# Kernel optimization log

Measured on AMD Instinct MI355X. Metric: run time of the kernel, lower is better.

## Reference

```python
import jax, jax.numpy as jnp
import numpy as np

B, S, D, H = 4, 2048, 1024, 16
HD = D // H


def setup_inputs() -> dict:
    key = jax.random.key(0)
    ks = jax.random.split(key, 12)
    sc = 1.0 / np.sqrt(D)
    return {
        "x": jax.random.normal(ks[0], (B, S, D), dtype=jnp.float32),
        "key_padding_mask": jax.random.randint(ks[1], (B, S), 0, 2).astype(bool),
        "attn_mask_modifier": jax.random.uniform(ks[2], (B, S, S), dtype=jnp.float32),
        "Wq": jax.random.normal(ks[3], (D, D), dtype=jnp.float32) * sc,
        "bq": jax.random.normal(ks[4], (D,), dtype=jnp.float32) * sc,
        "Wk": jax.random.normal(ks[5], (D, D), dtype=jnp.float32) * sc,
        "bk": jax.random.normal(ks[6], (D,), dtype=jnp.float32) * sc,
        "Wv": jax.random.normal(ks[7], (D, D), dtype=jnp.float32) * sc,
        "bv": jax.random.normal(ks[8], (D,), dtype=jnp.float32) * sc,
        "Wo": jax.random.normal(ks[9], (D, D), dtype=jnp.float32) * sc,
        "bo": jax.random.normal(ks[10], (D,), dtype=jnp.float32) * sc,
    }


def reference(x, key_padding_mask, attn_mask_modifier, Wq, bq, Wk, bk, Wv, bv, Wo, bo):
    b, s, d = x.shape
    hd = d // H
    # QKV projections -> [b, H, s, hd]
    q = (x @ Wq + bq).reshape(b, s, H, hd).transpose(0, 2, 1, 3)
    k = (x @ Wk + bk).reshape(b, s, H, hd).transpose(0, 2, 1, 3)
    v = (x @ Wv + bv).reshape(b, s, H, hd).transpose(0, 2, 1, 3)
    energy = jnp.einsum("bhqd,bhkd->bhqk", q, k) / jnp.sqrt(jnp.asarray(hd, x.dtype))
    # handle_neg=False path: multiplicative mask modifier, broadcast over heads
    energy = energy * attn_mask_modifier[:, None, :, :]
    # key_padding_mask is applied on the QUERY axis (unsqueeze(1).unsqueeze(-1)) per source
    energy = jnp.where(key_padding_mask[:, None, :, None], jnp.asarray(-1e10, x.dtype), energy)
    attn = jax.nn.softmax(energy, axis=-1)
    out = jnp.einsum("bhqk,bhkd->bhqd", attn, v).transpose(0, 2, 1, 3).reshape(b, s, d)
    return out @ Wo + bo
```

## Files before the change

### kernel.cpp

```cpp
#include <hip/hip_runtime.h>
#include <cstddef>

constexpr int Bn  = 4;
constexpr int Sn  = 2048;
constexpr int Dn  = 1024;
constexpr int Hn  = 16;
constexpr int HDn = 64;

typedef __bf16 bf16;
typedef __attribute__((ext_vector_type(8))) __bf16 bf16x8;
typedef __attribute__((ext_vector_type(4))) __bf16 bf16x4;
typedef __attribute__((ext_vector_type(4))) float  f32x4;

typedef __attribute__((address_space(1))) const void gvoid;
typedef __attribute__((address_space(3))) void lvoid;

__global__ __launch_bounds__(256) void conv_f32_bf16_k(
    const float* __restrict__ in, bf16* __restrict__ out, int n)
{
    int i = (blockIdx.x * 256 + threadIdx.x) * 4;
    if (i + 3 < n) {
        float4 v = *(const float4*)(in + i);
        bf16 o[4] = {(bf16)v.x, (bf16)v.y, (bf16)v.z, (bf16)v.w};
        *(ulong1*)(out + i) = *(ulong1*)o;
    }
}

__global__ __launch_bounds__(256) void conv_wt_k(
    const float* __restrict__ w0, const float* __restrict__ w1,
    const float* __restrict__ w2, const float* __restrict__ w3,
    bf16* __restrict__ o0, bf16* __restrict__ o1,
    bf16* __restrict__ o2, bf16* __restrict__ o3)
{
    const float* W = (blockIdx.z == 0) ? w0 : (blockIdx.z == 1) ? w1
                   : (blockIdx.z == 2) ? w2 : w3;
    bf16* O = (blockIdx.z == 0) ? o0 : (blockIdx.z == 1) ? o1
            : (blockIdx.z == 2) ? o2 : o3;
    __shared__ float t[64][65];
    const int tid = threadIdx.x;
    const int k0 = blockIdx.x * 64;
    const int n0 = blockIdx.y * 64;
    #pragma unroll
    for (int p = 0; p < 16; ++p) {
        const int idx = p * 256 + tid;
        const int r = idx >> 6, c = idx & 63;
        t[r][c] = W[(size_t)(k0 + r) * Dn + n0 + c];
    }
    __syncthreads();
    #pragma unroll
    for (int p = 0; p < 16; ++p) {
        const int idx = p * 256 + tid;
        const int r = idx >> 6, c = idx & 63;
        O[(size_t)(n0 + r) * Dn + k0 + c] = (bf16)t[c][r];
    }
}

template <int MODE>
__global__ __launch_bounds__(256) void gemm_bf16_k(
    const bf16* __restrict__ A, const bf16* __restrict__ Bt,
    const float* __restrict__ bias, void* __restrict__ outv)
{
    __shared__ __align__(16) bf16 As[128 * 64];
    __shared__ __align__(16) bf16 Bs[128 * 64];

    const int tid  = threadIdx.x;
    const int w    = tid >> 6;
    const int lane = tid & 63;
    const int quad = lane >> 4;
    const int l15  = lane & 15;
    const int m0   = blockIdx.x * 128;
    const int n0   = blockIdx.y * 128;
    const int wm   = w >> 1;
    const int wn   = w & 1;

    const int srow = lane >> 3;
    const int scol = (lane & 7) * 8;

    f32x4 acc[4][4] = {};

    for (int k0 = 0; k0 < Dn; k0 += 64) {
        #pragma unroll
        for (int j = 0; j < 4; ++j) {
            const int rbase = (w * 4 + j) * 8;
            const int r = rbase + srow;
            __builtin_amdgcn_global_load_lds(
                (gvoid*)(A + (size_t)(m0 + r) * Dn + k0 + scol),
                (lvoid*)&As[rbase * 64], 16, 0, 0);
            __builtin_amdgcn_global_load_lds(
                (gvoid*)(Bt + (size_t)(n0 + r) * Dn + k0 + scol),
                (lvoid*)&Bs[rbase * 64], 16, 0, 0);
        }
        __syncthreads();

        #pragma unroll
        for (int ks = 0; ks < 64; ks += 32) {
            bf16x8 af[4], bfr[4];
            #pragma unroll
            for (int fm = 0; fm < 4; ++fm)
                af[fm] = *(const bf16x8*)&As[(wm * 64 + fm * 16 + l15) * 64 + ks + quad * 8];
            #pragma unroll
            for (int fn = 0; fn < 4; ++fn)
                bfr[fn] = *(const bf16x8*)&Bs[(wn * 64 + fn * 16 + l15) * 64 + ks + quad * 8];
            #pragma unroll
            for (int fm = 0; fm < 4; ++fm)
                #pragma unroll
                for (int fn = 0; fn < 4; ++fn)
                    acc[fm][fn] = __builtin_amdgcn_mfma_f32_16x16x32_bf16(
                        af[fm], bfr[fn], acc[fm][fn], 0, 0, 0);
        }
        __syncthreads();
    }

    #pragma unroll
    for (int fn = 0; fn < 4; ++fn) {
        const int c = n0 + wn * 64 + fn * 16 + l15;
        const float bv = bias[c];
        #pragma unroll
        for (int fm = 0; fm < 4; ++fm) {
            #pragma unroll
            for (int i = 0; i < 4; ++i) {
                const int m = m0 + wm * 64 + fm * 16 + quad * 4 + i;
                const float v = acc[fm][fn][i] + bv;
                if (MODE == 0) {
                    ((float*)outv)[(size_t)m * Dn + c] = v;
                } else {
                    const int b = m >> 11, s = m & (Sn - 1);
                    const int h = c >> 6, hd = c & 63;
                    if (MODE == 1)
                        ((bf16*)outv)[(((size_t)(b * Hn + h) * Sn) + s) * HDn + hd] = (bf16)v;
                    else
                        ((bf16*)outv)[(((size_t)(b * Hn + h) * HDn) + hd) * Sn + s] = (bf16)v;
                }
            }
        }
    }
}

__device__ __forceinline__ int sidx(int r, int c) {
    return r * 64 + (c ^ ((r & 7) << 3));
}

__global__ __launch_bounds__(256) void attn_mfma_k(
    const bf16* __restrict__ Qb, const bf16* __restrict__ Kb,
    const bf16* __restrict__ Vtb, const int* __restrict__ kpm,
    const float* __restrict__ mod, bf16* __restrict__ att)
{
    __shared__ __align__(16) bf16 Ks[64 * 64];
    __shared__ __align__(16) bf16 Vts[64 * 64];
    __shared__ __align__(16) bf16 Ps[64 * 64];

    const int tid  = threadIdx.x;
    const int w    = tid >> 6;
    const int lane = tid & 63;
    const int quad = lane >> 4;
    const int l15  = lane & 15;
    const int blk  = blockIdx.x;
    const int bh   = blk >> 5;
    const int q0   = (blk & 31) * 64;
    const int b    = bh >> 4;
    const int h    = bh & 15;
    const size_t base = (size_t)bh * Sn * HDn;

    const int qrow = q0 + w * 16 + l15;
    const bf16x8 qf0 = *(const bf16x8*)(Qb + base + (size_t)qrow * HDn + 0  + quad * 8);
    const bf16x8 qf1 = *(const bf16x8*)(Qb + base + (size_t)qrow * HDn + 32 + quad * 8);

    const bool qm = kpm[(size_t)b * Sn + qrow] != 0;
    const float* modrow = mod + ((size_t)b * Sn + qrow) * Sn;

    constexpr float SC = 0.125f * 1.44269504088896340736f;

    float m_r = -1e30f;
    float l_r = 0.0f;
    f32x4 O[4] = {};

    int sr[2], soff[2];
    #pragma unroll
    for (int p = 0; p < 2; ++p) {
        const int c = p * 256 + tid;
        sr[p] = c >> 3; soff[p] = (c & 7) * 8;
    }

    bf16x8 kst[2], vst[2];
    float4 md[4];
    #pragma unroll
    for (int p = 0; p < 2; ++p) {
        kst[p] = *(const bf16x8*)(Kb + base + (size_t)sr[p] * HDn + soff[p]);
        vst[p] = *(const bf16x8*)(Vtb + base + (size_t)sr[p] * Sn + 0 + soff[p]);
    }
    #pragma unroll
    for (int ct = 0; ct < 4; ++ct)
        md[ct] = *(const float4*)(modrow + 0 + ct * 16 + quad * 4);
    #pragma unroll
    for (int p = 0; p < 2; ++p) {
        *(bf16x8*)&Ks[sidx(sr[p], soff[p])]  = kst[p];
        *(bf16x8*)&Vts[sidx(sr[p], soff[p])] = vst[p];
    }
    __syncthreads();

    constexpr int NT = Sn / 64;
    for (int t = 0; t < NT; ++t) {
        const int k0 = t * 64;

        float4 mdn[4];
        if (t + 1 < NT) {
            const int kn = k0 + 64;
            #pragma unroll
            for (int p = 0; p < 2; ++p) {
                kst[p] = *(const bf16x8*)(Kb + base + (size_t)(kn + sr[p]) * HDn + soff[p]);
                vst[p] = *(const bf16x8*)(Vtb + base + (size_t)sr[p] * Sn + kn + soff[p]);
            }
            #pragma unroll
            for (int ct = 0; ct < 4; ++ct)
                mdn[ct] = *(const float4*)(modrow + kn + ct * 16 + quad * 4);
        }

        float e[4][4];
        #pragma unroll
        for (int ct = 0; ct < 4; ++ct) {
            f32x4 s = {};
            #pragma unroll
            for (int ks = 0; ks < 64; ks += 32) {
                bf16x8 kf = *(const bf16x8*)&Ks[sidx(ct * 16 + l15, ks + quad * 8)];
                s = __builtin_amdgcn_mfma_f32_16x16x32_bf16(kf, ks ? qf1 : qf0, s, 0, 0, 0);
            }
            #pragma unroll
            for (int i = 0; i < 4; ++i)
                e[ct][i] = qm ? -1e10f : s[i] * SC * (&md[ct].x)[i];
        }

        float pmax = e[0][0];
        #pragma unroll
        for (int ct = 0; ct < 4; ++ct)
            #pragma unroll
            for (int i = 0; i < 4; ++i)
                pmax = fmaxf(pmax, e[ct][i]);
        pmax = fmaxf(pmax, __shfl_xor(pmax, 16));
        pmax = fmaxf(pmax, __shfl_xor(pmax, 32));

        const float mnew  = fmaxf(m_r, pmax);
        const float alpha = __builtin_amdgcn_exp2f(m_r - mnew);
        m_r = mnew;

        float rs = 0.0f;
        #pragma unroll
        for (int ct = 0; ct < 4; ++ct) {
            bf16x4 pb;
            #pragma unroll
            for (int i = 0; i < 4; ++i) {
                const bf16 p = (bf16)__builtin_amdgcn_exp2f(e[ct][i] - mnew);
                pb[i] = p;
                rs += (float)p;
            }
            *(bf16x4*)&Ps[sidx(w * 16 + l15, ct * 16 + quad * 4)] = pb;
        }
        rs += __shfl_xor(rs, 16);
        rs += __shfl_xor(rs, 32);
        l_r = l_r * alpha + rs;

        float aO[4];
        #pragma unroll
        for (int i = 0; i < 4; ++i)
            aO[i] = __shfl(alpha, quad * 4 + i, 16);
        #pragma unroll
        for (int ct = 0; ct < 4; ++ct)
            #pragma unroll
            for (int i = 0; i < 4; ++i)
                O[ct][i] *= aO[i];

        #pragma unroll
        for (int ks = 0; ks < 64; ks += 32) {
            bf16x8 paf = *(const bf16x8*)&Ps[sidx(w * 16 + l15, ks + quad * 8)];
            #pragma unroll
            for (int ct = 0; ct < 4; ++ct) {
                bf16x8 vf = *(const bf16x8*)&Vts[sidx(ct * 16 + l15, ks + quad * 8)];
                O[ct] = __builtin_amdgcn_mfma_f32_16x16x32_bf16(paf, vf, O[ct], 0, 0, 0);
            }
        }

        __syncthreads();
        if (t + 1 < NT) {
            #pragma unroll
            for (int p = 0; p < 2; ++p) {
                *(bf16x8*)&Ks[sidx(sr[p], soff[p])]  = kst[p];
                *(bf16x8*)&Vts[sidx(sr[p], soff[p])] = vst[p];
            }
            #pragma unroll
            for (int ct = 0; ct < 4; ++ct)
                md[ct] = mdn[ct];
        }
        __syncthreads();
    }

    float lO[4];
    #pragma unroll
    for (int i = 0; i < 4; ++i)
        lO[i] = 1.0f / __shfl(l_r, quad * 4 + i, 16);
    #pragma unroll
    for (int ct = 0; ct < 4; ++ct)
        #pragma unroll
        for (int i = 0; i < 4; ++i) {
            const int row = q0 + w * 16 + quad * 4 + i;
            const int col = h * HDn + ct * 16 + l15;
            att[((size_t)b * Sn + row) * Dn + col] = (bf16)(O[ct][i] * lO[i]);
        }
}

extern "C" void kernel_launch(void* const* d_in, const int* in_sizes, int n_in,
                              void* d_out, int out_size, void* d_ws, size_t ws_size,
                              hipStream_t stream) {
    const float* x   = (const float*)d_in[0];
    const int*   kpm = (const int*)d_in[1];
    const float* mod = (const float*)d_in[2];
    const float* Wq  = (const float*)d_in[3];
    const float* bq  = (const float*)d_in[4];
    const float* Wk  = (const float*)d_in[5];
    const float* bk  = (const float*)d_in[6];
    const float* Wv  = (const float*)d_in[7];
    const float* bv  = (const float*)d_in[8];
    const float* Wo  = (const float*)d_in[9];
    const float* bo  = (const float*)d_in[10];
    float* out = (float*)d_out;

    bf16* ws = (bf16*)d_ws;
    const size_t sz = (size_t)Bn * Sn * Dn;
    const size_t wz = (size_t)Dn * Dn;
    bf16* xb   = ws;
    bf16* qb   = ws + sz;
    bf16* kb   = ws + 2 * sz;
    bf16* vtb  = ws + 3 * sz;
    bf16* attb = ws + 4 * sz;
    bf16* wqt  = ws + 5 * sz;
    bf16* wkt  = wqt + wz;
    bf16* wvt  = wkt + wz;
    bf16* wot  = wvt + wz;

    conv_f32_bf16_k<<<(int)(sz / 1024), 256, 0, stream>>>(x, xb, (int)sz);
    conv_wt_k<<<dim3(16, 16, 4), 256, 0, stream>>>(Wq, Wk, Wv, Wo, wqt, wkt, wvt, wot);

    const dim3 gemm_grid(64, 8);
    gemm_bf16_k<1><<<gemm_grid, 256, 0, stream>>>(xb, wqt, bq, qb);
    gemm_bf16_k<1><<<gemm_grid, 256, 0, stream>>>(xb, wkt, bk, kb);
    gemm_bf16_k<2><<<gemm_grid, 256, 0, stream>>>(xb, wvt, bv, vtb);

    attn_mfma_k<<<Bn * Hn * (Sn / 64), 256, 0, stream>>>(qb, kb, vtb, kpm, mod, attb);

    gemm_bf16_k<0><<<gemm_grid, 256, 0, stream>>>(attb, wot, bo, out);
}
```

Baseline: 437.4 us.

## Double-buffer attention K/V via direct LDS loads, lazy rescale, fold scale into Q

The attention kernel now double-buffers K and V tiles in LDS, filling them with global_load_lds directly from memory instead of staging through registers, and drops one barrier per iteration. The online softmax rescales O and l only when the running max grows by more than a threshold (a conditional-rescale trick). The softmax scale is folded into the Q projection epilogue. The V-transpose GEMM epilogue now goes through an LDS transpose so global stores are coalesced. Risks: the direct LDS loads are not followed by an explicit vmcnt wait, and the removed barrier may create a race on the Ps buffer and on buffer reuse across iterations.

```diff
diff --git a/kernel.cpp b/kernel.cpp
--- a/kernel.cpp
+++ b/kernel.cpp
@@ -58,10 +58,12 @@
 template <int MODE>
 __global__ __launch_bounds__(256) void gemm_bf16_k(
     const bf16* __restrict__ A, const bf16* __restrict__ Bt,
-    const float* __restrict__ bias, void* __restrict__ outv)
+    const float* __restrict__ bias, void* __restrict__ outv, float scale)
 {
-    __shared__ __align__(16) bf16 As[128 * 64];
-    __shared__ __align__(16) bf16 Bs[128 * 64];
+    constexpr int SM_ELEMS = (MODE == 2) ? (128 * 136) : (2 * 128 * 64);
+    __shared__ __align__(16) bf16 smem[SM_ELEMS];
+    bf16* const As = smem;
+    bf16* const Bs = smem + 128 * 64;
 
     const int tid  = threadIdx.x;
     const int w    = tid >> 6;
@@ -111,25 +113,52 @@
         __syncthreads();
     }
 
-    #pragma unroll
-    for (int fn = 0; fn < 4; ++fn) {
-        const int c = n0 + wn * 64 + fn * 16 + l15;
-        const float bv = bias[c];
-        #pragma unroll
-        for (int fm = 0; fm < 4; ++fm) {
-            #pragma unroll
-            for (int i = 0; i < 4; ++i) {
-                const int m = m0 + wm * 64 + fm * 16 + quad * 4 + i;
-                const float v = acc[fm][fn][i] + bv;
-                if (MODE == 0) {
-                    ((float*)outv)[(size_t)m * Dn + c] = v;
-                } else {
-                    const int b = m >> 11, s = m & (Sn - 1);
-                    const int h = c >> 6, hd = c & 63;
-                    if (MODE == 1)
+    if (MODE == 2) {
+        bf16* const T = smem;
+        #pragma unroll
+        for (int fn = 0; fn < 4; ++fn) {
+            const int n = wn * 64 + fn * 16 + l15;
+            const float bv = bias[n0 + n];
+            #pragma unroll
+            for (int fm = 0; fm < 4; ++fm) {
+                const int m = wm * 64 + fm * 16 + quad * 4;
+                bf16x4 pk;
+                #pragma unroll
+                for (int i = 0; i < 4; ++i)
+                    pk[i] = (bf16)((acc[fm][fn][i] + bv) * scale);
+                *(bf16x4*)&T[n * 136 + m] = pk;
+            }
+        }
+        __syncthreads();
+        const int b  = m0 >> 11;
+        const int s0 = m0 & (Sn - 1);
+        #pragma unroll
+        for (int it = 0; it < 8; ++it) {
+            const int n    = it * 16 + (tid >> 4);
+            const int mcol = (tid & 15) * 8;
+            const int gh = (n0 + n) >> 6, ghd = (n0 + n) & 63;
+            bf16x8 v = *(const bf16x8*)&T[n * 136 + mcol];
+            *(bf16x8*)((bf16*)outv +
+                (((size_t)(b * Hn + gh) * HDn) + ghd) * Sn + s0 + mcol) = v;
+        }
+    } else {
+        #pragma unroll
+        for (int fn = 0; fn < 4; ++fn) {
+            const int c = n0 + wn * 64 + fn * 16 + l15;
+            const float bv = bias[c];
+            #pragma unroll
+            for (int fm = 0; fm < 4; ++fm) {
+                #pragma unroll
+                for (int i = 0; i < 4; ++i) {
+                    const int m = m0 + wm * 64 + fm * 16 + quad * 4 + i;
+                    const float v = (acc[fm][fn][i] + bv) * scale;
+                    if (MODE == 0) {
+                        ((float*)outv)[(size_t)m * Dn + c] = v;
+                    } else {
+                        const int b = m >> 11, s = m & (Sn - 1);
+                        const int h = c >> 6, hd = c & 63;
                         ((bf16*)outv)[(((size_t)(b * Hn + h) * Sn) + s) * HDn + hd] = (bf16)v;
-                    else
-                        ((bf16*)outv)[(((size_t)(b * Hn + h) * HDn) + hd) * Sn + s] = (bf16)v;
+                    }
                 }
             }
         }
@@ -145,8 +174,8 @@
     const bf16* __restrict__ Vtb, const int* __restrict__ kpm,
     const float* __restrict__ mod, bf16* __restrict__ att)
 {
-    __shared__ __align__(16) bf16 Ks[64 * 64];
-    __shared__ __align__(16) bf16 Vts[64 * 64];
+    __shared__ __align__(16) bf16 Ks[2][64 * 64];
+    __shared__ __align__(16) bf16 Vts[2][64 * 64];
     __shared__ __align__(16) bf16 Ps[64 * 64];
 
     const int tid  = threadIdx.x;
@@ -168,51 +197,44 @@
     const bool qm = kpm[(size_t)b * Sn + qrow] != 0;
     const float* modrow = mod + ((size_t)b * Sn + qrow) * Sn;
 
-    constexpr float SC = 0.125f * 1.44269504088896340736f;
-
     float m_r = -1e30f;
     float l_r = 0.0f;
     f32x4 O[4] = {};
 
-    int sr[2], soff[2];
-    #pragma unroll
-    for (int p = 0; p < 2; ++p) {
-        const int c = p * 256 + tid;
-        sr[p] = c >> 3; soff[p] = (c & 7) * 8;
-    }
-
-    bf16x8 kst[2], vst[2];
+    const int rl = lane >> 3;
+    const int cg = ((lane & 7) ^ rl) * 8;
+
+    auto stage = [&](int t, int buf) {
+        const int k0 = t * 64;
+        #pragma unroll
+        for (int p = 0; p < 2; ++p) {
+            const int gb = p * 32 + w * 8;
+            __builtin_amdgcn_global_load_lds(
+                (gvoid*)(Kb + base + (size_t)(k0 + gb + rl) * HDn + cg),
+                (lvoid*)&Ks[buf][gb * 64], 16, 0, 0);
+            __builtin_amdgcn_global_load_lds(
+                (gvoid*)(Vtb + base + (size_t)(gb + rl) * Sn + k0 + cg),
+                (lvoid*)&Vts[buf][gb * 64], 16, 0, 0);
+        }
+    };
+
+    stage(0, 0);
     float4 md[4];
     #pragma unroll
-    for (int p = 0; p < 2; ++p) {
-        kst[p] = *(const bf16x8*)(Kb + base + (size_t)sr[p] * HDn + soff[p]);
-        vst[p] = *(const bf16x8*)(Vtb + base + (size_t)sr[p] * Sn + 0 + soff[p]);
-    }
-    #pragma unroll
     for (int ct = 0; ct < 4; ++ct)
-        md[ct] = *(const float4*)(modrow + 0 + ct * 16 + quad * 4);
-    #pragma unroll
-    for (int p = 0; p < 2; ++p) {
-        *(bf16x8*)&Ks[sidx(sr[p], soff[p])]  = kst[p];
-        *(bf16x8*)&Vts[sidx(sr[p], soff[p])] = vst[p];
-    }
+        md[ct] = *(const float4*)(modrow + ct * 16 + quad * 4);
     __syncthreads();
 
     constexpr int NT = Sn / 64;
     for (int t = 0; t < NT; ++t) {
-        const int k0 = t * 64;
+        const int cur = t & 1;
 
         float4 mdn[4];
         if (t + 1 < NT) {
-            const int kn = k0 + 64;
-            #pragma unroll
-            for (int p = 0; p < 2; ++p) {
-                kst[p] = *(const bf16x8*)(Kb + base + (size_t)(kn + sr[p]) * HDn + soff[p]);
-                vst[p] = *(const bf16x8*)(Vtb + base + (size_t)sr[p] * Sn + kn + soff[p]);
-            }
+            stage(t + 1, cur ^ 1);
             #pragma unroll
             for (int ct = 0; ct < 4; ++ct)
-                mdn[ct] = *(const float4*)(modrow + kn + ct * 16 + quad * 4);
+                mdn[ct] = *(const float4*)(modrow + (t + 1) * 64 + ct * 16 + quad * 4);
         }
 
         float e[4][4];
@@ -221,12 +243,12 @@
             f32x4 s = {};
             #pragma unroll
             for (int ks = 0; ks < 64; ks += 32) {
-                bf16x8 kf = *(const bf16x8*)&Ks[sidx(ct * 16 + l15, ks + quad * 8)];
+                bf16x8 kf = *(const bf16x8*)&Ks[cur][sidx(ct * 16 + l15, ks + quad * 8)];
                 s = __builtin_amdgcn_mfma_f32_16x16x32_bf16(kf, ks ? qf1 : qf0, s, 0, 0, 0);
             }
             #pragma unroll
             for (int i = 0; i < 4; ++i)
-                e[ct][i] = qm ? -1e10f : s[i] * SC * (&md[ct].x)[i];
+                e[ct][i] = qm ? -1e10f : s[i] * (&md[ct].x)[i];
         }
 
         float pmax = e[0][0];
@@ -238,9 +260,21 @@
         pmax = fmaxf(pmax, __shfl_xor(pmax, 16));
         pmax = fmaxf(pmax, __shfl_xor(pmax, 32));
 
-        const float mnew  = fmaxf(m_r, pmax);
-        const float alpha = __builtin_amdgcn_exp2f(m_r - mnew);
-        m_r = mnew;
+        if (__any(pmax > m_r + 8.0f)) {
+            const float mnew  = fmaxf(m_r, pmax);
+            const float alpha = __builtin_amdgcn_exp2f(m_r - mnew);
+            m_r = mnew;
+            l_r *= alpha;
+            float aO[4];
+            #pragma unroll
+            for (int i = 0; i < 4; ++i)
+                aO[i] = __shfl(alpha, quad * 4 + i, 16);
+            #pragma unroll
+            for (int ct = 0; ct < 4; ++ct)
+                #pragma unroll
+                for (int i = 0; i < 4; ++i)
+                    O[ct][i] *= aO[i];
+        }
 
         float rs = 0.0f;
         #pragma unroll
@@ -248,7 +282,7 @@
             bf16x4 pb;
             #pragma unroll
             for (int i = 0; i < 4; ++i) {
-                const bf16 p = (bf16)__builtin_amdgcn_exp2f(e[ct][i] - mnew);
+                const bf16 p = (bf16)__builtin_amdgcn_exp2f(e[ct][i] - m_r);
                 pb[i] = p;
                 rs += (float)p;
             }
@@ -256,35 +290,19 @@
         }
         rs += __shfl_xor(rs, 16);
         rs += __shfl_xor(rs, 32);
-        l_r = l_r * alpha + rs;
-
-        float aO[4];
-        #pragma unroll
-        for (int i = 0; i < 4; ++i)
-            aO[i] = __shfl(alpha, quad * 4 + i, 16);
-        #pragma unroll
-        for (int ct = 0; ct < 4; ++ct)
-            #pragma unroll
-            for (int i = 0; i < 4; ++i)
-                O[ct][i] *= aO[i];
+        l_r += rs;
 
         #pragma unroll
         for (int ks = 0; ks < 64; ks += 32) {
             bf16x8 paf = *(const bf16x8*)&Ps[sidx(w * 16 + l15, ks + quad * 8)];
             #pragma unroll
             for (int ct = 0; ct < 4; ++ct) {
-                bf16x8 vf = *(const bf16x8*)&Vts[sidx(ct * 16 + l15, ks + quad * 8)];
+                bf16x8 vf = *(const bf16x8*)&Vts[cur][sidx(ct * 16 + l15, ks + quad * 8)];
                 O[ct] = __builtin_amdgcn_mfma_f32_16x16x32_bf16(paf, vf, O[ct], 0, 0, 0);
             }
         }
 
-        __syncthreads();
         if (t + 1 < NT) {
-            #pragma unroll
-            for (int p = 0; p < 2; ++p) {
-                *(bf16x8*)&Ks[sidx(sr[p], soff[p])]  = kst[p];
-                *(bf16x8*)&Vts[sidx(sr[p], soff[p])] = vst[p];
-            }
             #pragma unroll
             for (int ct = 0; ct < 4; ++ct)
                 md[ct] = mdn[ct];
@@ -338,12 +356,14 @@
     conv_f32_bf16_k<<<(int)(sz / 1024), 256, 0, stream>>>(x, xb, (int)sz);
     conv_wt_k<<<dim3(16, 16, 4), 256, 0, stream>>>(Wq, Wk, Wv, Wo, wqt, wkt, wvt, wot);
 
+    const float SC = 0.125f * 1.44269504088896340736f;
+
     const dim3 gemm_grid(64, 8);
-    gemm_bf16_k<1><<<gemm_grid, 256, 0, stream>>>(xb, wqt, bq, qb);
-    gemm_bf16_k<1><<<gemm_grid, 256, 0, stream>>>(xb, wkt, bk, kb);
-    gemm_bf16_k<2><<<gemm_grid, 256, 0, stream>>>(xb, wvt, bv, vtb);
+    gemm_bf16_k<1><<<gemm_grid, 256, 0, stream>>>(xb, wqt, bq, qb, SC);
+    gemm_bf16_k<1><<<gemm_grid, 256, 0, stream>>>(xb, wkt, bk, kb, 1.0f);
+    gemm_bf16_k<2><<<gemm_grid, 256, 0, stream>>>(xb, wvt, bv, vtb, 1.0f);
 
     attn_mfma_k<<<Bn * Hn * (Sn / 64), 256, 0, stream>>>(qb, kb, vtb, kpm, mod, attb);
 
-    gemm_bf16_k<0><<<gemm_grid, 256, 0, stream>>>(attb, wot, bo, out);
-}
+    gemm_bf16_k<0><<<gemm_grid, 256, 0, stream>>>(attb, wot, bo, out, 1.0f);
+}
```

Result: no change. 443.8 us (+1.5%).
